# Performance work log

Measured on AMD Instinct MI355X. Metric: run time of the kernel, lower is better.

## Reference

```python
import jax, jax.numpy as jnp
import numpy as np

FILTERS = 128

def setup_inputs() -> dict:
    key = jax.random.key(0)
    ks = jax.random.split(key, 8)
    B, Nq, Nkv, C = 4, 4096, 4096, 128
    q_inputs = jax.random.normal(ks[0], (B, Nq, C), dtype=jnp.float32)
    kv_inputs = jax.random.normal(ks[1], (B, Nkv, C), dtype=jnp.float32)
    s = 1.0 / np.sqrt(C)
    Wq = jax.random.normal(ks[2], (C, FILTERS), dtype=jnp.float32) * s
    Wk = jax.random.normal(ks[3], (C, FILTERS), dtype=jnp.float32) * s
    Wv = jax.random.normal(ks[4], (C, FILTERS), dtype=jnp.float32) * s
    bq = jnp.zeros((FILTERS,), jnp.float32)
    bk = jnp.zeros((FILTERS,), jnp.float32)
    bv = jnp.zeros((FILTERS,), jnp.float32)
    return {"q_inputs": q_inputs, "kv_inputs": kv_inputs,
            "Wq": Wq, "bq": bq, "Wk": Wk, "bk": bk, "Wv": Wv, "bv": bv}

def reference(q_inputs, kv_inputs, Wq, bq, Wk, bk, Wv, bv):
    # Dense projections (last-axis matmul + bias)
    q = jnp.einsum('bnc,cf->bnf', q_inputs, Wq) + bq
    k = jnp.einsum('bmc,cf->bmf', kv_inputs, Wk) + bk
    v = jnp.einsum('bmc,cf->bmf', kv_inputs, Wv) + bv
    scale = jnp.sqrt(jnp.asarray(FILTERS, jnp.float32))
    scores = jnp.einsum('bnf,bmf->bnm', q, k) / scale  # [B, Nq, Nkv]
    weights = jax.nn.softmax(scores, axis=-1)
    return jnp.einsum('bnm,bmf->bnf', weights, v)
```

## Files before the change

kernel.cpp:

```cpp
#include <hip/hip_runtime.h>
#include <stdint.h>

typedef unsigned short u16;
typedef __bf16 bf16x8 __attribute__((ext_vector_type(8)));
typedef unsigned short u16x8 __attribute__((ext_vector_type(8)));
typedef unsigned short u16x4 __attribute__((ext_vector_type(4)));
typedef float f32x4 __attribute__((ext_vector_type(4)));

#define MFMA16(a, b, c) __builtin_amdgcn_mfma_f32_16x16x32_bf16((a), (b), (c), 0, 0, 0)

__device__ __forceinline__ u16 f2b(float f) {
    union { unsigned int i; float f; } v; v.f = f;
    unsigned int r = (v.i + 0x7FFFu + ((v.i >> 16) & 1u)) >> 16;
    return (u16)r;
}

constexpr int N = 4096;
constexpr int Cc = 128;
constexpr int Fc = 128;
constexpr int BATCH = 4;

constexpr int XS_STRIDE = 136;
constexpr int WT_STRIDE = 136;
constexpr int KS_STRIDE = 136;
constexpr int VTS_STRIDE = 136;
constexpr int PS_STRIDE = 72;

__global__ __launch_bounds__(256) void wtrans_kernel(
    const float* __restrict__ Wq, const float* __restrict__ Wk,
    const float* __restrict__ Wv, u16* __restrict__ WtG)
{
    __shared__ __align__(16) u16 Wl[128 * 132];
    const int tid = threadIdx.x;
    const int which = blockIdx.x;
    const float* W = which == 0 ? Wq : (which == 1 ? Wk : Wv);
#pragma unroll
    for (int it = 0; it < 16; ++it) {
        int idx4 = tid + it * 256; int e0 = idx4 * 4;
        int c = e0 >> 7, f = e0 & 127;
        float4 wv = *(const float4*)(W + e0);
        u16x4 h; h[0] = f2b(wv.x); h[1] = f2b(wv.y); h[2] = f2b(wv.z); h[3] = f2b(wv.w);
        *(u16x4*)&Wl[c * 132 + f] = h;
    }
    __syncthreads();
    u16* out = WtG + which * 16384;
#pragma unroll
    for (int it = 0; it < 8; ++it) {
        int idx8 = tid + it * 256; int e0 = idx8 * 8;
        int f = e0 >> 7, c = e0 & 127;
        u16x8 h;
#pragma unroll
        for (int j = 0; j < 8; ++j) h[j] = Wl[(c + j) * 132 + f];
        *(u16x8*)(out + e0) = h;
    }
}

__global__ __launch_bounds__(256) void proj_kernel(
    const float* __restrict__ q_in, const float* __restrict__ kv_in,
    const u16* __restrict__ WtG,
    const float* __restrict__ bq, const float* __restrict__ bk,
    const float* __restrict__ bv,
    u16* __restrict__ Qw, u16* __restrict__ Kw, u16* __restrict__ Vtw)
{
    __shared__ __align__(16) u16 Xs[64 * XS_STRIDE];
    __shared__ __align__(16) u16 Wt[128 * WT_STRIDE];

    const int tid = threadIdx.x;
    const int which = blockIdx.y;
    const int b = blockIdx.z;
    const int m0 = blockIdx.x * 64;

    const float* X = (which == 0 ? q_in : kv_in) + ((size_t)b * N + m0) * Cc;
    const u16* Wsrc = WtG + which * 16384;
    const float* bias = which == 0 ? bq : (which == 1 ? bk : bv);

#pragma unroll
    for (int it = 0; it < 8; ++it) {
        int idx4 = tid + it * 256; int e0 = idx4 * 4;
        int r = e0 >> 7, c = e0 & 127;
        float4 xv = *(const float4*)(X + e0);
        u16x4 h; h[0] = f2b(xv.x); h[1] = f2b(xv.y); h[2] = f2b(xv.z); h[3] = f2b(xv.w);
        *(u16x4*)&Xs[r * XS_STRIDE + c] = h;
    }
#pragma unroll
    for (int it = 0; it < 8; ++it) {
        int idx8 = tid + it * 256; int e0 = idx8 * 8;
        int f = e0 >> 7, c = e0 & 127;
        *(u16x8*)&Wt[f * WT_STRIDE + c] = *(const u16x8*)(Wsrc + e0);
    }
    __syncthreads();

    const int lane = tid & 63;
    const int w = tid >> 6;
    const int n16 = lane & 15;
    const int quad = lane >> 4;

    if (which < 2) {
        bf16x8 ax[4];
#pragma unroll
        for (int kk = 0; kk < 4; ++kk)
            ax[kk] = *(const bf16x8*)&Xs[(w * 16 + n16) * XS_STRIDE + kk * 32 + quad * 8];
        const float scale = (which == 0) ? 0.08838834764831845f : 1.0f;
        u16* Out = (which == 0) ? Qw : Kw;
#pragma unroll
        for (int ft = 0; ft < 8; ++ft) {
            f32x4 acc = {0.f, 0.f, 0.f, 0.f};
#pragma unroll
            for (int kk = 0; kk < 4; ++kk) {
                bf16x8 bw = *(const bf16x8*)&Wt[(ft * 16 + n16) * WT_STRIDE + kk * 32 + quad * 8];
                acc = MFMA16(ax[kk], bw, acc);
            }
            float bias_f = bias[ft * 16 + n16];
#pragma unroll
            for (int r = 0; r < 4; ++r) {
                int row = m0 + w * 16 + quad * 4 + r;
                Out[((size_t)b * N + row) * Fc + ft * 16 + n16] = f2b((acc[r] + bias_f) * scale);
            }
        }
    } else {
#pragma unroll
        for (int ft2 = 0; ft2 < 2; ++ft2) {
            int ftg = w * 2 + ft2;
            bf16x8 aw[4];
#pragma unroll
            for (int kk = 0; kk < 4; ++kk)
                aw[kk] = *(const bf16x8*)&Wt[(ftg * 16 + n16) * WT_STRIDE + kk * 32 + quad * 8];
            float bias4[4];
#pragma unroll
            for (int r = 0; r < 4; ++r) bias4[r] = bias[ftg * 16 + quad * 4 + r];
#pragma unroll
            for (int nt = 0; nt < 4; ++nt) {
                f32x4 acc = {0.f, 0.f, 0.f, 0.f};
#pragma unroll
                for (int kk = 0; kk < 4; ++kk) {
                    bf16x8 bx = *(const bf16x8*)&Xs[(nt * 16 + n16) * XS_STRIDE + kk * 32 + quad * 8];
                    acc = MFMA16(aw[kk], bx, acc);
                }
#pragma unroll
                for (int r = 0; r < 4; ++r) {
                    int fg = ftg * 16 + quad * 4 + r;
                    int rowg = m0 + nt * 16 + n16;
                    Vtw[((size_t)b * Fc + fg) * N + rowg] = f2b(acc[r] + bias4[r]);
                }
            }
        }
    }
}

__global__ __launch_bounds__(512, 2) void attn_kernel(
    const u16* __restrict__ Qw, const u16* __restrict__ Kw,
    const u16* __restrict__ Vtw, float* __restrict__ out)
{
    __shared__ __align__(16) u16 smem[2 * 128 * KS_STRIDE + 2 * 128 * VTS_STRIDE + 8 * 16 * PS_STRIDE];
    u16* Kbuf = smem;
    u16* Vbuf = smem + 2 * 128 * KS_STRIDE;
    u16* Ps   = Vbuf + 2 * 128 * VTS_STRIDE;

    const int tid = threadIdx.x;
    const int b = blockIdx.y;
    const int q0 = blockIdx.x * 64;
    const int lane = tid & 63;
    const int w = tid >> 6;
    const int wq = w & 3;
    const int grp = w >> 2;
    const int n16 = lane & 15;
    const int quad = lane >> 4;

    bf16x8 aq[4];
    {
        const u16* qrow = Qw + ((size_t)b * N + q0 + wq * 16 + n16) * Cc;
#pragma unroll
        for (int kk = 0; kk < 4; ++kk)
            aq[kk] = *(const bf16x8*)(qrow + kk * 32 + quad * 8);
    }

    int rr[4], cc[4];
#pragma unroll
    for (int it = 0; it < 4; ++it) {
        int idx8 = tid + it * 512; int e0 = idx8 * 8;
        rr[it] = e0 >> 7; cc[it] = e0 & 127;
    }
    const u16* Kbase = Kw + (size_t)b * N * Cc;
    const u16* Vbase = Vtw + (size_t)b * Fc * N;

    u16x8 kreg[4], vreg[4];
#pragma unroll
    for (int it = 0; it < 4; ++it) {
        kreg[it] = *(const u16x8*)(Kbase + (size_t)rr[it] * Cc + cc[it]);
        vreg[it] = *(const u16x8*)(Vbase + (size_t)rr[it] * N + cc[it]);
    }

    f32x4 o[8];
#pragma unroll
    for (int ct = 0; ct < 8; ++ct) o[ct] = (f32x4){0.f, 0.f, 0.f, 0.f};
    float lloc = 0.f;

    u16* Psw = Ps + w * 16 * PS_STRIDE;

    for (int t = 0; t < N / 128; ++t) {
        u16* Ks  = Kbuf + (t & 1) * 128 * KS_STRIDE;
        u16* Vts = Vbuf + (t & 1) * 128 * VTS_STRIDE;

#pragma unroll
        for (int it = 0; it < 4; ++it) {
            *(u16x8*)&Ks[rr[it] * KS_STRIDE + cc[it]] = kreg[it];
            *(u16x8*)&Vts[rr[it] * VTS_STRIDE + cc[it]] = vreg[it];
        }
        __syncthreads();

        if (t + 1 < N / 128) {
            int k0n = (t + 1) * 128;
#pragma unroll
            for (int it = 0; it < 4; ++it) {
                kreg[it] = *(const u16x8*)(Kbase + (size_t)(k0n + rr[it]) * Cc + cc[it]);
                vreg[it] = *(const u16x8*)(Vbase + (size_t)rr[it] * N + k0n + cc[it]);
            }
        }

        f32x4 st[4];
#pragma unroll
        for (int kt = 0; kt < 4; ++kt) {
            f32x4 acc = {0.f, 0.f, 0.f, 0.f};
#pragma unroll
            for (int kk = 0; kk < 4; ++kk) {
                bf16x8 ak = *(const bf16x8*)&Ks[(grp * 64 + kt * 16 + n16) * KS_STRIDE + kk * 32 + quad * 8];
                acc = MFMA16(ak, aq[kk], acc);
            }
            st[kt] = acc;
        }

#pragma unroll
        for (int kt = 0; kt < 4; ++kt) {
            float e0 = __expf(st[kt][0]), e1 = __expf(st[kt][1]);
            float e2 = __expf(st[kt][2]), e3 = __expf(st[kt][3]);
            lloc += (e0 + e1) + (e2 + e3);
            u16x4 pk; pk[0] = f2b(e0); pk[1] = f2b(e1); pk[2] = f2b(e2); pk[3] = f2b(e3);
            *(u16x4*)&Psw[n16 * PS_STRIDE + kt * 16 + quad * 4] = pk;
        }

        bf16x8 pa[2];
#pragma unroll
        for (int kch = 0; kch < 2; ++kch)
            pa[kch] = *(const bf16x8*)&Psw[n16 * PS_STRIDE + kch * 32 + quad * 8];
#pragma unroll
        for (int ct = 0; ct < 8; ++ct) {
#pragma unroll
            for (int kch = 0; kch < 2; ++kch) {
                bf16x8 bv_ = *(const bf16x8*)&Vts[(ct * 16 + n16) * VTS_STRIDE + grp * 64 + kch * 32 + quad * 8];
                o[ct] = MFMA16(pa[kch], bv_, o[ct]);
            }
        }
    }
    __syncthreads();

    float lv = lloc;
    lv += __shfl_xor(lv, 16);
    lv += __shfl_xor(lv, 32);

    float* Om = (float*)smem;
    float* Lm = Om + 64 * 132;
    if (grp == 1) {
#pragma unroll
        for (int ct = 0; ct < 8; ++ct)
#pragma unroll
            for (int r = 0; r < 4; ++r)
                Om[(wq * 16 + quad * 4 + r) * 132 + ct * 16 + n16] = o[ct][r];
        if (lane < 16) Lm[wq * 16 + n16] = lv;
    }
    __syncthreads();
    if (grp == 0) {
        float lsum[4];
#pragma unroll
        for (int r = 0; r < 4; ++r)
            lsum[r] = __shfl(lv, quad * 4 + r) + Lm[wq * 16 + quad * 4 + r];
#pragma unroll
        for (int ct = 0; ct < 8; ++ct) {
#pragma unroll
            for (int r = 0; r < 4; ++r) {
                int q = q0 + wq * 16 + quad * 4 + r;
                float ov = o[ct][r] + Om[(wq * 16 + quad * 4 + r) * 132 + ct * 16 + n16];
                out[((size_t)b * N + q) * Fc + ct * 16 + n16] = ov / lsum[r];
            }
        }
    }
}

extern "C" void kernel_launch(void* const* d_in, const int* in_sizes, int n_in,
                              void* d_out, int out_size, void* d_ws, size_t ws_size,
                              hipStream_t stream) {
    (void)in_sizes; (void)n_in; (void)out_size; (void)ws_size;
    const float* q_in  = (const float*)d_in[0];
    const float* kv_in = (const float*)d_in[1];
    const float* Wq = (const float*)d_in[2];
    const float* bq = (const float*)d_in[3];
    const float* Wk = (const float*)d_in[4];
    const float* bk = (const float*)d_in[5];
    const float* Wv = (const float*)d_in[6];
    const float* bv = (const float*)d_in[7];

    const size_t qkv = (size_t)BATCH * N * Fc;
    u16* Qw  = (u16*)d_ws;
    u16* Kw  = Qw + qkv;
    u16* Vtw = Kw + qkv;
    u16* WtG = Vtw + qkv;

    wtrans_kernel<<<dim3(3), dim3(256), 0, stream>>>(Wq, Wk, Wv, WtG);
    proj_kernel<<<dim3(64, 3, BATCH), dim3(256), 0, stream>>>(
        q_in, kv_in, WtG, bq, bk, bv, Qw, Kw, Vtw);
    attn_kernel<<<dim3(64, BATCH), dim3(512), 0, stream>>>(
        Qw, Kw, Vtw, (float*)d_out);
}
```

Before: 147.6 us.

## Switch attention kernel to 32x32x16 MFMA with 4-way KV split per query tile

```diff
diff --git a/kernel.cpp b/kernel.cpp
--- a/kernel.cpp
+++ b/kernel.cpp
@@ -6,8 +6,10 @@
 typedef unsigned short u16x8 __attribute__((ext_vector_type(8)));
 typedef unsigned short u16x4 __attribute__((ext_vector_type(4)));
 typedef float f32x4 __attribute__((ext_vector_type(4)));
+typedef float f32x16 __attribute__((ext_vector_type(16)));
 
 #define MFMA16(a, b, c) __builtin_amdgcn_mfma_f32_16x16x32_bf16((a), (b), (c), 0, 0, 0)
+#define MFMA32(a, b, c) __builtin_amdgcn_mfma_f32_32x32x16_bf16((a), (b), (c), 0, 0, 0)
 
 __device__ __forceinline__ u16 f2b(float f) {
     union { unsigned int i; float f; } v; v.f = f;
@@ -24,7 +26,7 @@
 constexpr int WT_STRIDE = 136;
 constexpr int KS_STRIDE = 136;
 constexpr int VTS_STRIDE = 136;
-constexpr int PS_STRIDE = 72;
+constexpr int PS2_STRIDE = 40;
 
 __global__ __launch_bounds__(256) void wtrans_kernel(
     const float* __restrict__ Wq, const float* __restrict__ Wk,
@@ -151,7 +153,7 @@
     const u16* __restrict__ Qw, const u16* __restrict__ Kw,
     const u16* __restrict__ Vtw, float* __restrict__ out)
 {
-    __shared__ __align__(16) u16 smem[2 * 128 * KS_STRIDE + 2 * 128 * VTS_STRIDE + 8 * 16 * PS_STRIDE];
+    __shared__ __align__(16) u16 smem[2 * 128 * KS_STRIDE + 2 * 128 * VTS_STRIDE + 8 * 32 * PS2_STRIDE];
     u16* Kbuf = smem;
     u16* Vbuf = smem + 2 * 128 * KS_STRIDE;
     u16* Ps   = Vbuf + 2 * 128 * VTS_STRIDE;
@@ -161,17 +163,17 @@
     const int q0 = blockIdx.x * 64;
     const int lane = tid & 63;
     const int w = tid >> 6;
-    const int wq = w & 3;
-    const int grp = w >> 2;
-    const int n16 = lane & 15;
-    const int quad = lane >> 4;
-
-    bf16x8 aq[4];
+    const int grp = w & 3;
+    const int qg = w >> 2;
+    const int l31 = lane & 31;
+    const int l5 = lane >> 5;
+
+    bf16x8 aq[8];
     {
-        const u16* qrow = Qw + ((size_t)b * N + q0 + wq * 16 + n16) * Cc;
-#pragma unroll
-        for (int kk = 0; kk < 4; ++kk)
-            aq[kk] = *(const bf16x8*)(qrow + kk * 32 + quad * 8);
+        const u16* qrow = Qw + ((size_t)b * N + q0 + qg * 32 + l31) * Cc;
+#pragma unroll
+        for (int k = 0; k < 8; ++k)
+            aq[k] = *(const bf16x8*)(qrow + k * 16 + 8 * l5);
     }
 
     int rr[4], cc[4];
@@ -190,12 +192,14 @@
         vreg[it] = *(const u16x8*)(Vbase + (size_t)rr[it] * N + cc[it]);
     }
 
-    f32x4 o[8];
-#pragma unroll
-    for (int ct = 0; ct < 8; ++ct) o[ct] = (f32x4){0.f, 0.f, 0.f, 0.f};
+    f32x16 o[4];
+#pragma unroll
+    for (int ct = 0; ct < 4; ++ct)
+#pragma unroll
+        for (int e = 0; e < 16; ++e) o[ct][e] = 0.f;
     float lloc = 0.f;
 
-    u16* Psw = Ps + w * 16 * PS_STRIDE;
+    u16* Psw = Ps + w * 32 * PS2_STRIDE;
 
     for (int t = 0; t < N / 128; ++t) {
         u16* Ks  = Kbuf + (t & 1) * 128 * KS_STRIDE;
@@ -217,69 +221,69 @@
             }
         }
 
-        f32x4 st[4];
-#pragma unroll
-        for (int kt = 0; kt < 4; ++kt) {
-            f32x4 acc = {0.f, 0.f, 0.f, 0.f};
-#pragma unroll
-            for (int kk = 0; kk < 4; ++kk) {
-                bf16x8 ak = *(const bf16x8*)&Ks[(grp * 64 + kt * 16 + n16) * KS_STRIDE + kk * 32 + quad * 8];
-                acc = MFMA16(ak, aq[kk], acc);
-            }
-            st[kt] = acc;
-        }
-
-#pragma unroll
-        for (int kt = 0; kt < 4; ++kt) {
-            float e0 = __expf(st[kt][0]), e1 = __expf(st[kt][1]);
-            float e2 = __expf(st[kt][2]), e3 = __expf(st[kt][3]);
+        f32x16 st;
+#pragma unroll
+        for (int e = 0; e < 16; ++e) st[e] = 0.f;
+#pragma unroll
+        for (int k = 0; k < 8; ++k) {
+            bf16x8 ak = *(const bf16x8*)&Ks[(grp * 32 + l31) * KS_STRIDE + k * 16 + 8 * l5];
+            st = MFMA32(ak, aq[k], st);
+        }
+
+#pragma unroll
+        for (int rq = 0; rq < 4; ++rq) {
+            float e0 = __expf(st[4 * rq + 0]), e1 = __expf(st[4 * rq + 1]);
+            float e2 = __expf(st[4 * rq + 2]), e3 = __expf(st[4 * rq + 3]);
             lloc += (e0 + e1) + (e2 + e3);
             u16x4 pk; pk[0] = f2b(e0); pk[1] = f2b(e1); pk[2] = f2b(e2); pk[3] = f2b(e3);
-            *(u16x4*)&Psw[n16 * PS_STRIDE + kt * 16 + quad * 4] = pk;
-        }
-
-        bf16x8 pa[2];
-#pragma unroll
-        for (int kch = 0; kch < 2; ++kch)
-            pa[kch] = *(const bf16x8*)&Psw[n16 * PS_STRIDE + kch * 32 + quad * 8];
-#pragma unroll
-        for (int ct = 0; ct < 8; ++ct) {
-#pragma unroll
-            for (int kch = 0; kch < 2; ++kch) {
-                bf16x8 bv_ = *(const bf16x8*)&Vts[(ct * 16 + n16) * VTS_STRIDE + grp * 64 + kch * 32 + quad * 8];
-                o[ct] = MFMA16(pa[kch], bv_, o[ct]);
+            *(u16x4*)&Psw[l31 * PS2_STRIDE + 8 * rq + 4 * l5] = pk;
+        }
+
+#pragma unroll
+        for (int ks = 0; ks < 2; ++ks) {
+            bf16x8 pa = *(const bf16x8*)&Psw[l31 * PS2_STRIDE + ks * 16 + 8 * l5];
+#pragma unroll
+            for (int ct = 0; ct < 4; ++ct) {
+                bf16x8 bv_ = *(const bf16x8*)&Vts[(ct * 32 + l31) * VTS_STRIDE + grp * 32 + ks * 16 + 8 * l5];
+                o[ct] = MFMA32(pa, bv_, o[ct]);
             }
         }
     }
     __syncthreads();
 
     float lv = lloc;
-    lv += __shfl_xor(lv, 16);
     lv += __shfl_xor(lv, 32);
 
     float* Om = (float*)smem;
-    float* Lm = Om + 64 * 132;
-    if (grp == 1) {
-#pragma unroll
-        for (int ct = 0; ct < 8; ++ct)
-#pragma unroll
-            for (int r = 0; r < 4; ++r)
-                Om[(wq * 16 + quad * 4 + r) * 132 + ct * 16 + n16] = o[ct][r];
-        if (lane < 16) Lm[wq * 16 + n16] = lv;
+    float* Lm = Om + 3 * 64 * 132;
+    if (grp != 0) {
+        int qb = (grp - 1) * 64 + qg * 32;
+#pragma unroll
+        for (int ct = 0; ct < 4; ++ct)
+#pragma unroll
+            for (int reg = 0; reg < 16; ++reg) {
+                int qr = (reg & 3) + 8 * (reg >> 2) + 4 * l5;
+                Om[(qb + qr) * 132 + ct * 32 + l31] = o[ct][reg];
+            }
+        if (lane < 32) Lm[(grp - 1) * 64 + qg * 32 + l31] = lv;
     }
     __syncthreads();
     if (grp == 0) {
-        float lsum[4];
-#pragma unroll
-        for (int r = 0; r < 4; ++r)
-            lsum[r] = __shfl(lv, quad * 4 + r) + Lm[wq * 16 + quad * 4 + r];
-#pragma unroll
-        for (int ct = 0; ct < 8; ++ct) {
-#pragma unroll
-            for (int r = 0; r < 4; ++r) {
-                int q = q0 + wq * 16 + quad * 4 + r;
-                float ov = o[ct][r] + Om[(wq * 16 + quad * 4 + r) * 132 + ct * 16 + n16];
-                out[((size_t)b * N + q) * Fc + ct * 16 + n16] = ov / lsum[r];
+#pragma unroll
+        for (int reg = 0; reg < 16; ++reg) {
+            int qr = (reg & 3) + 8 * (reg >> 2) + 4 * l5;
+            float ls = __shfl(lv, qr);
+#pragma unroll
+            for (int j = 0; j < 3; ++j)
+                ls += Lm[j * 64 + qg * 32 + qr];
+            int q = q0 + qg * 32 + qr;
+#pragma unroll
+            for (int ct = 0; ct < 4; ++ct) {
+                float ov = o[ct][reg];
+#pragma unroll
+                for (int j = 0; j < 3; ++j)
+                    ov += Om[(j * 64 + qg * 32 + qr) * 132 + ct * 32 + l31];
+                out[((size_t)b * N + q) * Fc + ct * 32 + l31] = ov / ls;
             }
         }
     }
```

Result: faster. 139.1 us (-5.7%).
